# Kernel tuning notes

Measured on AMD Instinct MI355X. Metric: run time of the kernel, lower is better.

## Reference

```python
import jax, jax.numpy as jnp
import numpy as np

TOLX = 1e-12
TOLFUN = 1e-06
MAXITER = 1000
ALPHA = 1e-4
MIN_LAMBDA = 0.1
MAX_LAMBDA = 0.5
MAX_STEPS = 10  # fixed unroll budget; Newton converges in < 10 iterations for this problem
BS, NY = 200000, 8


def setup_inputs():
    key = jax.random.key(0)
    k1, k2, k3 = jax.random.split(key, 3)
    y0 = jax.random.normal(k1, (BS, NY), dtype=jnp.float32)
    W = 0.1 * jax.random.normal(k2, (NY, NY), dtype=jnp.float32)
    V = 0.1 * jax.random.normal(k3, (NY, NY), dtype=jnp.float32)
    dt = jnp.asarray(0.1, dtype=jnp.float32)
    t = jnp.asarray(1.0, dtype=jnp.float32)
    return {"y0": y0, "dt": dt, "t": t, "W": W, "V": V}


def _safe_div(n, d, eps=1e-30):
    ok = jnp.abs(d) > eps
    return jnp.where(ok, n / jnp.where(ok, d, 1.0), 0.0)


def _solver(y0, dt, t, W, V):
    bs, ny = y0.shape
    one = jnp.float32(1.0)

    def delta_S(tt, y):
        # test ODE right-hand side g(t, y): mildly nonlinear, acts per-sample
        return jnp.tanh(y @ W) @ V - 0.1 * y + 0.01 * jnp.sin(tt)

    def err(y):  # implicit-Euler residual, (bs, ny)
        return (y - y0) / dt - delta_S(t, y)

    def _err_single(yb, y0b):
        return (yb - y0b) / dt - (jnp.tanh(yb @ W) @ V - 0.1 * yb + 0.01 * jnp.sin(t))

    def batched_jac(y):
        # (bs, ny, ny): d err_b / d y_b; matches torch batch-diagonal of autograd jacobian
        return jax.vmap(jax.jacfwd(_err_single), in_axes=(0, 0))(y, y0)

    F0 = err(y0)
    jac0 = batched_jac(y0)
    rn0 = jnp.max(jnp.abs(F0), axis=1)
    fobj0 = jnp.einsum('bi,bi->b', F0, F0)

    state0 = dict(y=y0, yold=y0, F=F0, dy=jnp.zeros_like(y0), jac=jac0,
                  resnorm=rn0, resnorm0=100.0 * rn0,
                  lam=one, lam1=one, lam2=jnp.float32(0.5),
                  fold=fobj0, f2=fobj0, slope=jnp.zeros((bs,), y0.dtype),
                  lam_min=jnp.float32(0.0), niter=jnp.int32(0), exitflag=jnp.int32(1))

    def body(s, _):
        active = (((jnp.max(s['resnorm']) > TOLFUN) | (s['lam'] < 1.0))
                  & (s['exitflag'] >= 0) & (s['niter'] <= MAXITER))

        # --- lam == 1: fresh Newton direction, slope, objective ---
        is_newton = s['lam'] == 1.0
        recompute = jnp.max(_safe_div(s['resnorm'], s['resnorm0'])) > 0.2
        fresh_jac = batched_jac(s['y'])
        jac = jnp.where(is_newton & recompute, fresh_jac, s['jac'])
        dy_n = -jnp.linalg.solve(jac, s['F'][..., None])[..., 0]  # lstsq on square == solve
        gvec = jnp.einsum('bi,bij->bj', s['F'], jac)
        slope_n = jnp.einsum('bj,bj->b', gvec, dy_n)
        fold_n = jnp.einsum('bi,bi->b', s['F'], s['F'])
        lam_min_n = _safe_div(jnp.float32(TOLX),
                              jnp.max(jnp.abs(dy_n) / jnp.maximum(jnp.abs(s['y']), 1.0)))

        dy = jnp.where(is_newton, dy_n, s['dy'])
        slope = jnp.where(is_newton, slope_n, s['slope'])
        fold = jnp.where(is_newton, fold_n, s['fold'])
        yold = jnp.where(is_newton, s['y'], s['yold'])
        lam_min = jnp.where(is_newton, lam_min_n, s['lam_min'])
        niter = jnp.where(is_newton, s['niter'] + 1, s['niter'])

        brk = s['lam'] < lam_min            # -> exitflag = 2, freeze state
        bad = ~jnp.all(jnp.isfinite(dy))    # -> exitflag = -1, freeze state

        # --- trial step + trust-region line search ---
        lam = s['lam']
        y_new = yold + dy * lam
        F_new = err(y_new)
        f_obj = jnp.einsum('bi,bi->b', F_new, F_new)
        lam1 = lam
        lam2, f2 = s['lam2'], s['f2']

        backtrack = jnp.any(f_obj > fold + ALPHA * lam * slope)
        # quadratic model (first backtrack)
        lam_quad = jnp.min(_safe_div(-slope / 2.0, f_obj - fold - slope))
        # cubic model (subsequent backtracks)
        A = _safe_div(one, lam1 - lam2)
        inv1 = _safe_div(one, lam1 * lam1)
        inv2 = _safe_div(one, lam2 * lam2)
        B = jnp.stack([jnp.stack([inv1, -inv2]), jnp.stack([-lam2 * inv1, lam1 * inv2])])
        C = jnp.stack([f_obj - fold - lam1 * slope, f2 - fold - lam2 * slope])  # (2, bs)
        ab = A * (B @ C)
        a, b = ab[0], ab[1]
        disc = b * b - 3.0 * a * slope
        sq = jnp.sqrt(jnp.maximum(disc, 0.0))
        lam_tmp = jnp.where(jnp.all(a == 0.0), _safe_div(-slope, 2.0 * b),
                   jnp.where(jnp.any(disc < 0.0), MAX_LAMBDA * lam1,
                    jnp.where(jnp.any(b <= 0.0), _safe_div(-b + sq, 3.0 * a),
                     _safe_div(-slope, b + sq))))
        lam_cubic = jnp.min(jnp.minimum(lam_tmp, MAX_LAMBDA * lam1))
        lam_bt = jnp.where(lam == 1.0, lam_quad, lam_cubic)
        nanf = ~jnp.all(jnp.isfinite(f_obj))
        lam_new = jnp.where(backtrack, lam_bt, jnp.where(nanf, MAX_LAMBDA * lam1, one))

        cont = lam_new < 1.0  # retry with smaller lambda next iteration (the `continue` path)
        lam2_new = jnp.where(cont, lam1, lam2)
        f2_new = jnp.where(cont, f_obj, f2)
        lam_new = jnp.where(cont, jnp.maximum(lam_new, MIN_LAMBDA * lam1), lam_new)
        resnorm_new = jnp.where(cont, s['resnorm'], jnp.max(jnp.abs(F_new), axis=1))
        resnorm0_new = jnp.where(cont, s['resnorm0'], s['resnorm'])

        upd = active & (~brk) & (~bad)
        exitflag = jnp.where(active & brk, jnp.int32(2),
                    jnp.where(active & (~brk) & bad, jnp.int32(-1), s['exitflag']))
        sel = lambda new, old: jnp.where(upd, new, old)

        ns = dict(y=sel(y_new, s['y']), yold=sel(yold, s['yold']), F=sel(F_new, s['F']),
                  dy=sel(dy, s['dy']), jac=sel(jac, s['jac']),
                  resnorm=sel(resnorm_new, s['resnorm']), resnorm0=sel(resnorm0_new, s['resnorm0']),
                  lam=sel(lam_new, s['lam']), lam1=sel(lam1, s['lam1']), lam2=sel(lam2_new, s['lam2']),
                  fold=sel(fold, s['fold']), f2=sel(f2_new, s['f2']), slope=sel(slope, s['slope']),
                  lam_min=sel(lam_min, s['lam_min']),
                  niter=jnp.where(active, niter, s['niter']), exitflag=exitflag)
        return ns, None

    sN, _ = jax.lax.scan(body, state0, None, length=MAX_STEPS)
    return sN['y'], sN['F'], sN['exitflag']


def reference(y0, dt, t, W, V):
    y, F, exitflag = _solver(y0, dt, t, W, V)
    return (y, F, exitflag)
```

## Files before the change

### kernel.cpp

```cpp
#include <hip/hip_runtime.h>
#include <hip/hip_cooperative_groups.h>

namespace cg = cooperative_groups;

#define BSZ 200000
#define NSTEPS 10
#define TOLFUN_C 1e-6f
#define ALPHA_C 1e-4f

#define CNTHR 256
#define CNBLK 256
#define CNT   (CNBLK*CNTHR)
#define SPT   4
#define SLOTS (CNTHR*SPT)

#define FNTHR 256
#define FNBLK ((BSZ + FNTHR - 1)/FNTHR)

#define OFF_Y     ((size_t)0)
#define OFF_YOLD  ((size_t)BSZ*8)
#define OFF_DY    ((size_t)BSZ*16)
#define OFF_SJ    ((size_t)BSZ*24)
#define OFF_FOLD  ((size_t)BSZ*32)
#define OFF_SLOPE ((size_t)BSZ*33)
#define OFF_RESN  ((size_t)BSZ*34)
#define OFF_F2    ((size_t)BSZ*35)
#define OFF_TFO   ((size_t)BSZ*36)
#define OFF_TRN   ((size_t)BSZ*37)
#define OFF_R     ((size_t)BSZ*38)

#define RSTRIDE 64
#define NSLOT   9
#define R_TOT   (2 + NSTEPS*NSLOT)
#define KEY_MAX_IDENT 0x007FFFFFu
#define KEY_MIN_IDENT 0xFF800000u

static __device__ __forceinline__ float nanmax2(float a, float b){
    return (__builtin_isnan(a) || __builtin_isnan(b)) ? __builtin_nanf("") : fmaxf(a, b);
}
static __device__ __forceinline__ float nanmin2(float a, float b){
    return (__builtin_isnan(a) || __builtin_isnan(b)) ? __builtin_nanf("") : fminf(a, b);
}
static __device__ __forceinline__ float safe_div(float n, float d){
    return (fabsf(d) > 1e-30f) ? (n / d) : 0.0f;
}
static __device__ __forceinline__ unsigned fkey(float x){
    unsigned u = __float_as_uint(x);
    return (u & 0x80000000u) ? ~u : (u | 0x80000000u);
}
static __device__ __forceinline__ float funkey(unsigned u){
    return (u & 0x80000000u) ? __uint_as_float(u & 0x7FFFFFFFu) : __uint_as_float(~u);
}
static __device__ __forceinline__ unsigned fkey_max(float x){
    if (__builtin_isnan(x)) x = __uint_as_float(0x7FC00000u);
    return fkey(x);
}
static __device__ __forceinline__ unsigned fkey_min(float x){
    if (__builtin_isnan(x)) x = __uint_as_float(0xFFC00000u);
    return fkey(x);
}
static __device__ __forceinline__ void ld8(const float* p, float* v){
    float4 a = ((const float4*)p)[0], b = ((const float4*)p)[1];
    v[0]=a.x; v[1]=a.y; v[2]=a.z; v[3]=a.w; v[4]=b.x; v[5]=b.y; v[6]=b.z; v[7]=b.w;
}
static __device__ __forceinline__ void st8(float* p, const float* v){
    float4 a, b;
    a.x=v[0]; a.y=v[1]; a.z=v[2]; a.w=v[3];
    b.x=v[4]; b.y=v[5]; b.z=v[6]; b.w=v[7];
    ((float4*)p)[0]=a; ((float4*)p)[1]=b;
}
static __device__ __forceinline__ unsigned ldslot(const unsigned* p){
    return __hip_atomic_load(p, __ATOMIC_RELAXED, __HIP_MEMORY_SCOPE_AGENT);
}
static __device__ __forceinline__ void stslot(unsigned* p, unsigned v){
    __hip_atomic_store(p, v, __ATOMIC_RELAXED, __HIP_MEMORY_SCOPE_AGENT);
}

static __device__ __forceinline__ void computeFz(
    const float* yv, const float* y0v, float dt, float c0,
    const float* sW, const float* sV, float* Fo, float* zo)
{
    float u[8];
    #pragma unroll
    for (int k=0;k<8;k++){
        float acc = 0.f;
        #pragma unroll
        for (int m=0;m<8;m++) acc += yv[m]*sW[m*8+k];
        u[k]=acc;
    }
    #pragma unroll
    for (int k=0;k<8;k++) zo[k] = tanhf(u[k]);
    #pragma unroll
    for (int i=0;i<8;i++){
        float tv = 0.f;
        #pragma unroll
        for (int k=0;k<8;k++) tv += zo[k]*sV[k*8+i];
        Fo[i] = (yv[i]-y0v[i])/dt - ((tv - 0.1f*yv[i]) + c0);
    }
}

static __device__ __forceinline__ void devInit2(const float* y0v,
    float* yold, float* dy, float* sj,
    float& fold_o, float& slope_o, float& resn_o, float& f2_o,
    float dt, float c0, const float* sW, const float* sV,
    float& rn_red, float& rat_red)
{
    #pragma unroll
    for (int i=0;i<8;i++){ yold[i]=y0v[i]; dy[i]=0.f; }
    float Fv[8], z[8];
    computeFz(y0v, y0v, dt, c0, sW, sV, Fv, z);
    #pragma unroll
    for (int k=0;k<8;k++) sj[k] = 1.0f - z[k]*z[k];
    float fold = 0.f;
    #pragma unroll
    for (int i=0;i<8;i++) fold += Fv[i]*Fv[i];
    float rn0 = fabsf(Fv[0]);
    #pragma unroll
    for (int i=1;i<8;i++) rn0 = nanmax2(rn0, fabsf(Fv[i]));
    fold_o=fold; slope_o=0.f; resn_o=rn0; f2_o=fold;
    rn_red  = nanmax2(rn_red, rn0);
    rat_red = nanmax2(rat_red, safe_div(rn0, 100.0f*rn0));
}

static __device__ __forceinline__ void devA2(const float* y_cur, const float* y0v,
    float* yold, float* dy, float* sj, float& fold_o, float& slope_o,
    float dt, float invdt, float c0, const float* sW, const float* sV,
    bool recompute, float& gml, bool& nf)
{
    float Fv[8], z[8];
    computeFz(y_cur, y0v, dt, c0, sW, sV, Fv, z);
    if (recompute){
        #pragma unroll
        for (int k=0;k<8;k++) sj[k] = 1.0f - z[k]*z[k];
    }
    float J[8][8];
    #pragma unroll
    for (int j=0;j<8;j++){
        float zj[8];
        #pragma unroll
        for (int k=0;k<8;k++) zj[k] = sW[j*8+k]*sj[k];
        #pragma unroll
        for (int i=0;i<8;i++){
            float acc = 0.f;
            #pragma unroll
            for (int k=0;k<8;k++) acc += zj[k]*sV[k*8+i];
            J[i][j] = (i==j) ? (invdt - (acc - 0.1f)) : (0.0f - acc);
        }
    }
    float fold = 0.f;
    #pragma unroll
    for (int i=0;i<8;i++) fold += Fv[i]*Fv[i];
    float gv[8];
    #pragma unroll
    for (int j=0;j<8;j++){
        float acc = 0.f;
        #pragma unroll
        for (int i=0;i<8;i++) acc += Fv[i]*J[i][j];
        gv[j]=acc;
    }
    float x[8];
    #pragma unroll
    for (int i=0;i<8;i++) x[i]=Fv[i];
    #pragma unroll
    for (int c=0;c<8;c++){
        float ip = 1.0f / J[c][c];
        #pragma unroll
        for (int r2=c+1;r2<8;r2++){
            float m = J[r2][c]*ip;
            #pragma unroll
            for (int jj=c+1;jj<8;jj++) J[r2][jj] -= m*J[c][jj];
            x[r2] -= m*x[c];
        }
    }
    float wv[8];
    #pragma unroll
    for (int c=7;c>=0;c--){
        float acc = x[c];
        #pragma unroll
        for (int jj=c+1;jj<8;jj++) acc -= J[c][jj]*wv[jj];
        wv[c] = acc / J[c][c];
    }
    #pragma unroll
    for (int i=0;i<8;i++){
        yold[i] = y_cur[i];
        dy[i]   = -wv[i];
    }
    float slope = 0.f;
    #pragma unroll
    for (int j=0;j<8;j++) slope += gv[j]*dy[j];
    fold_o = fold; slope_o = slope;
    #pragma unroll
    for (int i=0;i<8;i++){
        float rr = fabsf(dy[i]) / nanmax2(fabsf(y_cur[i]), 1.0f);
        gml = nanmax2(gml, rr);
        nf = nf || !__builtin_isfinite(dy[i]);
    }
}

static __device__ __forceinline__ void devB2(const float* yold, const float* dy,
    const float* y0v, float foldv, float slopev, float resnv, float f2v,
    float dt, float c0, const float* sW, const float* sV, float lam, float lam2v,
    float& tfo_o, float& trn_o,
    bool& armijo, float& lq, bool& aNot0, bool& dN, bool& ble,
    float& mX, float& mZ, float& mW, bool& nanf, float& trnR, float& ratR)
{
    float yn[8];
    #pragma unroll
    for (int i=0;i<8;i++) yn[i] = yold[i] + dy[i]*lam;
    float Ft[8], z[8];
    computeFz(yn, y0v, dt, c0, sW, sV, Ft, z);
    float f_obj = 0.f;
    #pragma unroll
    for (int i=0;i<8;i++) f_obj += Ft[i]*Ft[i];
    float rn = fabsf(Ft[0]);
    #pragma unroll
    for (int i=1;i<8;i++) rn = nanmax2(rn, fabsf(Ft[i]));
    tfo_o = f_obj; trn_o = rn;
    armijo = armijo || (f_obj > (foldv + (ALPHA_C*lam)*slopev));
    lq = nanmin2(lq, safe_div((-slopev)*0.5f, (f_obj - foldv) - slopev));
    float lam1v = lam;
    float Af = safe_div(1.0f, lam1v - lam2v);
    float i1 = safe_div(1.0f, lam1v*lam1v);
    float i2 = safe_div(1.0f, lam2v*lam2v);
    float Cc0 = (f_obj - foldv) - lam1v*slopev;
    float Cc1 = (f2v   - foldv) - lam2v*slopev;
    float av = Af*(i1*Cc0 - i2*Cc1);
    float bv = Af*((-(lam2v*i1))*Cc0 + (lam1v*i2)*Cc1);
    float disc = bv*bv - (3.0f*av)*slopev;
    float dm = __builtin_isnan(disc) ? disc : fmaxf(disc, 0.0f);
    float sq = sqrtf(dm);
    aNot0 = aNot0 || (av != 0.0f);
    dN    = dN    || (disc < 0.0f);
    ble   = ble   || (bv <= 0.0f);
    mX = nanmin2(mX, safe_div(-slopev, 2.0f*bv));
    mZ = nanmin2(mZ, safe_div(-bv + sq, 3.0f*av));
    mW = nanmin2(mW, safe_div(-slopev, bv + sq));
    nanf = nanf || !__builtin_isfinite(f_obj);
    trnR = nanmax2(trnR, rn);
    ratR = nanmax2(ratR, safe_div(rn, resnv));
}

struct ScalarState {
    float lam, lam1, lam2, lam_min, maxrn, ratmax;
    int   niter, exitflag;
    bool  upd_prev, cont_prev;
};

static __device__ void advance(ScalarState& s, const unsigned* R, int j){
    const unsigned* r = R + (size_t)(2 + j*NSLOT)*RSTRIDE;
    unsigned v0 = ldslot(r + (size_t)0*RSTRIDE);
    unsigned v1 = ldslot(r + (size_t)1*RSTRIDE);
    unsigned v2 = ldslot(r + (size_t)2*RSTRIDE);
    unsigned v3 = ldslot(r + (size_t)3*RSTRIDE);
    unsigned v4 = ldslot(r + (size_t)4*RSTRIDE);
    unsigned v5 = ldslot(r + (size_t)5*RSTRIDE);
    unsigned v6 = ldslot(r + (size_t)6*RSTRIDE);
    unsigned v7 = ldslot(r + (size_t)7*RSTRIDE);
    unsigned v8 = ldslot(r + (size_t)8*RSTRIDE);
    bool active    = ((s.maxrn > TOLFUN_C) || (s.lam < 1.0f)) && (s.exitflag >= 0) && (s.niter <= 1000);
    bool is_newton = (s.lam == 1.0f);
    float lam_min_new = is_newton ? safe_div(1e-12f, funkey(v0)) : s.lam_min;
    bool brk = (s.lam < lam_min_new);
    bool bad = is_newton ? (v1 != 0u) : false;
    bool upd = active && !brk && !bad;
    int niter_new = active ? (is_newton ? s.niter + 1 : s.niter) : s.niter;
    int ef_new = s.exitflag;
    if (active && brk) ef_new = 2;
    else if (active && !brk && bad) ef_new = -1;
    bool cont = false;
    if (upd){
        float lam1c = s.lam;
        unsigned bm = v8;
        bool backtrack = (bm & 1u) != 0u;
        float lamq  = funkey(v2);
        bool allA0  = (bm & 2u) == 0u;
        bool anyDN  = (bm & 4u) != 0u;
        bool anyB0  = (bm & 8u) != 0u;
        float lam_tmp_min = allA0 ? funkey(v3)
                          : (anyDN ? (0.5f*lam1c)
                          : (anyB0 ? funkey(v4) : funkey(v5)));
        float lam_cubic = nanmin2(lam_tmp_min, 0.5f*lam1c);
        float lam_bt = (s.lam == 1.0f) ? lamq : lam_cubic;
        bool nanf = (bm & 16u) != 0u;
        float lam_new = backtrack ? lam_bt : (nanf ? 0.5f*lam1c : 1.0f);
        cont = (lam_new < 1.0f);
        float lam2_new = cont ? lam1c : s.lam2;
        if (cont) lam_new = nanmax2(lam_new, 0.1f*lam1c);
        float maxrn_new  = cont ? s.maxrn  : funkey(v6);
        float ratmax_new = cont ? s.ratmax : funkey(v7);
        s.lam = lam_new; s.lam1 = lam1c; s.lam2 = lam2_new;
        s.lam_min = lam_min_new; s.maxrn = maxrn_new; s.ratmax = ratmax_new;
    }
    s.niter = niter_new; s.exitflag = ef_new;
    s.upd_prev = upd; s.cont_prev = cont;
}

static __device__ ScalarState replayN(const unsigned* R, int n){
    ScalarState s;
    s.lam=1.0f; s.lam1=1.0f; s.lam2=0.5f; s.lam_min=0.0f;
    s.maxrn  = funkey(ldslot(&R[0]));
    s.ratmax = funkey(ldslot(&R[(size_t)1*RSTRIDE]));
    s.niter=0; s.exitflag=1; s.upd_prev=false; s.cont_prev=false;
    for (int j=0;j<n;++j) advance(s, R, j);
    return s;
}

__global__ __launch_bounds__(CNTHR, 1) void kFused(
    const float* __restrict__ y0g, const float* __restrict__ Wm, const float* __restrict__ Vm,
    const float* __restrict__ dtp, const float* __restrict__ tp,
    float* __restrict__ ws, float* __restrict__ out)
{
    cg::grid_group gridg = cg::this_grid();
    __shared__ float sW[64], sV[64];
    __shared__ float sSJ[8*SLOTS];
    __shared__ float redF[6][4];
    __shared__ unsigned redB[4];
    int t = threadIdx.x;
    if (t < 64) sW[t] = Wm[t];
    else if (t < 128) sV[t-64] = Vm[t-64];
    unsigned* R = (unsigned*)(ws + OFF_R);
    if (blockIdx.x == 0 && t < R_TOT){
        unsigned v;
        if (t < 2) v = KEY_MAX_IDENT;
        else {
            int off = (t - 2) % NSLOT;
            bool ismin = (off==2 || off==3 || off==4 || off==5);
            bool ismax = (off==0 || off==6 || off==7);
            v = ismin ? KEY_MIN_IDENT : (ismax ? KEY_MAX_IDENT : 0u);
        }
        stslot(&R[(size_t)t*RSTRIDE], v);
    }
    __syncthreads();
    gridg.sync();

    int gtid = blockIdx.x*CNTHR + t;
    float dt = *dtp, invdt = 1.0f/dt, c0 = 0.01f*sinf(*tp);

    bool  valid[SPT];
    float yold[SPT][8], dyv[SPT][8];
    float foldv[SPT], slopev[SPT], resnv[SPT], f2v[SPT], tfov[SPT], trnv[SPT];
    float lamc = 0.0f;

    float rn_red = -__builtin_inff(), rat_red = -__builtin_inff();
    #pragma unroll
    for (int q=0;q<SPT;q++){
        int sid = gtid + q*CNT;
        int slot = q*CNTHR + t;
        valid[q] = sid < BSZ;
        if (valid[q]){
            float y0v[8], sjl[8];
            ld8(y0g + (size_t)sid*8, y0v);
            devInit2(y0v, yold[q], dyv[q], sjl,
                     foldv[q], slopev[q], resnv[q], f2v[q],
                     dt, c0, sW, sV, rn_red, rat_red);
            #pragma unroll
            for (int i=0;i<8;i++) sSJ[i*SLOTS + slot] = sjl[i];
            tfov[q]=0.f; trnv[q]=0.f;
        } else {
            #pragma unroll
            for (int i=0;i<8;i++){ sSJ[i*SLOTS + slot]=0; yold[q][i]=0; dyv[q][i]=0; }
            foldv[q]=0; slopev[q]=0; resnv[q]=0; f2v[q]=0; tfov[q]=0; trnv[q]=0;
        }
    }
    #pragma unroll
    for (int o=32;o>=1;o>>=1){
        rn_red  = nanmax2(rn_red,  __shfl_xor(rn_red,  o, 64));
        rat_red = nanmax2(rat_red, __shfl_xor(rat_red, o, 64));
    }
    {
        int w = t >> 6;
        if ((t & 63) == 0){ redF[0][w] = rn_red; redF[1][w] = rat_red; }
        __syncthreads();
        if (t == 0){
            float a = redF[0][0];
            #pragma unroll
            for (int w2=1;w2<4;w2++) a = nanmax2(a, redF[0][w2]);
            atomicMax(&R[0], fkey_max(a));
        } else if (t == 1){
            float b = redF[1][0];
            #pragma unroll
            for (int w2=1;w2<4;w2++) b = nanmax2(b, redF[1][w2]);
            atomicMax(&R[(size_t)1*RSTRIDE], fkey_max(b));
        }
    }
    gridg.sync();

    ScalarState S;
    S.lam=1.0f; S.lam1=1.0f; S.lam2=0.5f; S.lam_min=0.0f;
    S.maxrn  = funkey(ldslot(&R[0]));
    S.ratmax = funkey(ldslot(&R[(size_t)1*RSTRIDE]));
    S.niter=0; S.exitflag=1; S.upd_prev=false; S.cont_prev=false;

    #pragma unroll 1
    for (int k=1; k<=NSTEPS; ++k){
        if (S.upd_prev){
            lamc = S.lam1;
            #pragma unroll
            for (int q=0;q<SPT;q++){
                if (!valid[q]) continue;
                if (S.cont_prev) f2v[q]  = tfov[q];
                else             resnv[q] = trnv[q];
            }
        }
        bool active    = ((S.maxrn > TOLFUN_C) || (S.lam < 1.0f)) && (S.exitflag >= 0) && (S.niter <= 1000);
        bool is_newton = (S.lam == 1.0f);
        unsigned* r = R + (size_t)(2 + (k-1)*NSLOT)*RSTRIDE;

        if (active && is_newton){
            bool recompute = (S.ratmax > 0.2f);
            float gml = -__builtin_inff(); bool nf = false;
            #pragma unroll
            for (int q=0;q<SPT;q++){
                if (!valid[q]) continue;
                int sid = gtid + q*CNT;
                int slot = q*CNTHR + t;
                float y_cur[8], y0v[8], sjl[8];
                ld8(y0g + (size_t)sid*8, y0v);
                #pragma unroll
                for (int i=0;i<8;i++){
                    y_cur[i] = yold[q][i] + dyv[q][i]*lamc;
                    sjl[i]   = sSJ[i*SLOTS + slot];
                }
                devA2(y_cur, y0v, yold[q], dyv[q], sjl, foldv[q], slopev[q],
                      dt, invdt, c0, sW, sV, recompute, gml, nf);
                if (recompute){
                    #pragma unroll
                    for (int i=0;i<8;i++) sSJ[i*SLOTS + slot] = sjl[i];
                }
            }
            lamc = 0.0f;
            #pragma unroll
            for (int o=32;o>=1;o>>=1) gml = nanmax2(gml, __shfl_xor(gml, o, 64));
            unsigned long long anym = __ballot(nf ? 1 : 0);
            int w = t >> 6;
            if ((t & 63) == 0){ redF[0][w] = gml; redB[w] = anym ? 1u : 0u; }
            __syncthreads();
            if (t == 0){
                float v = redF[0][0];
                #pragma unroll
                for (int w2=1;w2<4;w2++) v = nanmax2(v, redF[0][w2]);
                atomicMax(&r[0], fkey_max(v));
            } else if (t == 1){
                unsigned bm = redB[0]|redB[1]|redB[2]|redB[3];
                if (bm) atomicOr(&r[(size_t)1*RSTRIDE], 1u);
            }
            __syncthreads();
        }

        if (active){
            float lam = S.lam, lam2v = S.lam2;
            bool armijo=false, aNot0=false, dN=false, ble=false, nanf=false;
            float lq=__builtin_inff(), mX=__builtin_inff(), mZ=__builtin_inff(), mW=__builtin_inff();
            float trnR=-__builtin_inff(), ratR=-__builtin_inff();
            #pragma unroll
            for (int q=0;q<SPT;q++){
                if (!valid[q]) continue;
                int sid = gtid + q*CNT;
                float y0v[8];
                ld8(y0g + (size_t)sid*8, y0v);
                devB2(yold[q], dyv[q], y0v, foldv[q], slopev[q], resnv[q], f2v[q],
                      dt, c0, sW, sV, lam, lam2v, tfov[q], trnv[q],
                      armijo, lq, aNot0, dN, ble, mX, mZ, mW, nanf, trnR, ratR);
            }
            #pragma unroll
            for (int o=32;o>=1;o>>=1){
                lq   = nanmin2(lq,   __shfl_xor(lq,   o, 64));
                mX   = nanmin2(mX,   __shfl_xor(mX,   o, 64));
                mZ   = nanmin2(mZ,   __shfl_xor(mZ,   o, 64));
                mW   = nanmin2(mW,   __shfl_xor(mW,   o, 64));
                trnR = nanmax2(trnR, __shfl_xor(trnR, o, 64));
                ratR = nanmax2(ratR, __shfl_xor(ratR, o, 64));
            }
            unsigned long long bArm = __ballot(armijo ? 1 : 0);
            unsigned long long bA0  = __ballot(aNot0  ? 1 : 0);
            unsigned long long bDN  = __ballot(dN     ? 1 : 0);
            unsigned long long bB0  = __ballot(ble    ? 1 : 0);
            unsigned long long bNF  = __ballot(nanf   ? 1 : 0);
            int w = t >> 6;
            if ((t & 63) == 0){
                redF[0][w]=lq; redF[1][w]=mX; redF[2][w]=mZ; redF[3][w]=mW;
                redF[4][w]=trnR; redF[5][w]=ratR;
                redB[w] = (bArm?1u:0u) | (bA0?2u:0u) | (bDN?4u:0u) | (bB0?8u:0u) | (bNF?16u:0u);
            }
            __syncthreads();
            if (t < 6){
                float v = redF[t][0];
                bool ismin = (t < 4);
                #pragma unroll
                for (int w2=1;w2<4;w2++) v = ismin ? nanmin2(v, redF[t][w2]) : nanmax2(v, redF[t][w2]);
                unsigned* p = &r[(size_t)(t + 2)*RSTRIDE];
                if (ismin) atomicMin(p, fkey_min(v));
                else       atomicMax(p, fkey_max(v));
            } else if (t == 6){
                unsigned bm = redB[0]|redB[1]|redB[2]|redB[3];
                if (bm) atomicOr(&r[(size_t)8*RSTRIDE], bm);
            }
        }

        gridg.sync();
        advance(S, R, k-1);
    }

    if (S.upd_prev) lamc = S.lam1;
    #pragma unroll
    for (int q=0;q<SPT;q++){
        if (!valid[q]) continue;
        int sid = gtid + q*CNT;
        float yf[8], y0v[8];
        ld8(y0g + (size_t)sid*8, y0v);
        #pragma unroll
        for (int i=0;i<8;i++) yf[i] = yold[q][i] + dyv[q][i]*lamc;
        st8(out + (size_t)sid*8, yf);
        float Fv[8], z[8];
        computeFz(yf, y0v, dt, c0, sW, sV, Fv, z);
        st8(out + (size_t)BSZ*8 + (size_t)sid*8, Fv);
    }
    if (gtid == 0) out[(size_t)BSZ*16] = (float)S.exitflag;
}

__global__ void kPre(unsigned* __restrict__ R){
    int i = threadIdx.x;
    if (i >= R_TOT) return;
    unsigned v;
    if (i < 2) v = KEY_MAX_IDENT;
    else {
        int off = (i - 2) % NSLOT;
        bool ismin = (off==2 || off==3 || off==4 || off==5);
        bool ismax = (off==0 || off==6 || off==7);
        v = ismin ? KEY_MIN_IDENT : (ismax ? KEY_MAX_IDENT : 0u);
    }
    R[(size_t)i*RSTRIDE] = v;
}

__global__ __launch_bounds__(FNTHR) void fInit(
    const float* __restrict__ y0g, const float* __restrict__ Wm, const float* __restrict__ Vm,
    const float* __restrict__ dtp, const float* __restrict__ tp, float* __restrict__ ws)
{
    __shared__ float sW[64], sV[64];
    __shared__ float red[2][4];
    int t = threadIdx.x;
    if (t < 64) sW[t] = Wm[t];
    else if (t < 128) sV[t-64] = Vm[t-64];
    __syncthreads();
    unsigned* R = (unsigned*)(ws + OFF_R);
    int tid = blockIdx.x*FNTHR + t;
    bool valid = tid < BSZ;
    float dt = *dtp, c0 = 0.01f*sinf(*tp);
    float rn_red = -__builtin_inff(), rat_red = -__builtin_inff();
    if (valid){
        float y0v[8], yo[8], dv[8], sj[8], fold, slope, resn, f2;
        ld8(y0g + (size_t)tid*8, y0v);
        devInit2(y0v, yo, dv, sj, fold, slope, resn, f2, dt, c0, sW, sV, rn_red, rat_red);
        st8(ws+OFF_Y   +(size_t)tid*8, y0v);
        st8(ws+OFF_YOLD+(size_t)tid*8, yo);
        st8(ws+OFF_DY  +(size_t)tid*8, dv);
        st8(ws+OFF_SJ  +(size_t)tid*8, sj);
        ws[OFF_FOLD+tid]=fold; ws[OFF_SLOPE+tid]=slope;
        ws[OFF_RESN+tid]=resn; ws[OFF_F2+tid]=f2;
        ws[OFF_TFO+tid]=0.f;   ws[OFF_TRN+tid]=0.f;
    }
    #pragma unroll
    for (int o=32;o>=1;o>>=1){
        rn_red  = nanmax2(rn_red,  __shfl_xor(rn_red,  o, 64));
        rat_red = nanmax2(rat_red, __shfl_xor(rat_red, o, 64));
    }
    int w = t >> 6;
    if ((t & 63) == 0){ red[0][w]=rn_red; red[1][w]=rat_red; }
    __syncthreads();
    if (t == 0){
        float a = red[0][0];
        for (int w2=1;w2<4;w2++) a = nanmax2(a, red[0][w2]);
        atomicMax(&R[0], fkey_max(a));
    } else if (t == 1){
        float b = red[1][0];
        for (int w2=1;w2<4;w2++) b = nanmax2(b, red[1][w2]);
        atomicMax(&R[(size_t)1*RSTRIDE], fkey_max(b));
    }
}

__global__ __launch_bounds__(FNTHR) void fStep(
    const float* __restrict__ y0g, const float* __restrict__ Wm, const float* __restrict__ Vm,
    const float* __restrict__ dtp, const float* __restrict__ tp,
    float* __restrict__ ws, int step)
{
    __shared__ float sW[64], sV[64];
    __shared__ float redF[6][4];
    __shared__ unsigned redB[4];
    int t = threadIdx.x;
    if (t < 64) sW[t] = Wm[t];
    else if (t < 128) sV[t-64] = Vm[t-64];
    __syncthreads();
    unsigned* R = (unsigned*)(ws + OFF_R);
    ScalarState S = replayN(R, step-1);
    bool active    = ((S.maxrn > TOLFUN_C) || (S.lam < 1.0f)) && (S.exitflag >= 0) && (S.niter <= 1000);
    bool is_newton = (S.lam == 1.0f);
    if (!S.upd_prev && !active) return;

    int tid = blockIdx.x*FNTHR + t;
    bool valid = tid < BSZ;
    float dt = *dtp, invdt = 1.0f/dt, c0 = 0.01f*sinf(*tp);
    unsigned* r = R + (size_t)(2 + (step-1)*NSLOT)*RSTRIDE;

    float y0v[8], yv[8], yo[8], dv[8], sj[8], fold=0, slope=0, resn=0, f2=0;
    if (valid){
        ld8(y0g + (size_t)tid*8, y0v);
        ld8(ws+OFF_Y   +(size_t)tid*8, yv);
        ld8(ws+OFF_YOLD+(size_t)tid*8, yo);
        ld8(ws+OFF_DY  +(size_t)tid*8, dv);
        ld8(ws+OFF_SJ  +(size_t)tid*8, sj);
        fold=ws[OFF_FOLD+tid]; slope=ws[OFF_SLOPE+tid];
        resn=ws[OFF_RESN+tid]; f2=ws[OFF_F2+tid];
        if (S.upd_prev){
            #pragma unroll
            for (int i=0;i<8;i++) yv[i] = yo[i] + dv[i]*S.lam1;
            st8(ws+OFF_Y+(size_t)tid*8, yv);
            if (S.cont_prev){ f2 = ws[OFF_TFO+tid];  ws[OFF_F2+tid]   = f2; }
            else            { resn = ws[OFF_TRN+tid]; ws[OFF_RESN+tid] = resn; }
        }
    }
    if (!active) return;

    if (is_newton){
        bool recompute = (S.ratmax > 0.2f);
        float gml = -__builtin_inff(); bool nf = false;
        if (valid){
            devA2(yv, y0v, yo, dv, sj, fold, slope, dt, invdt, c0, sW, sV, recompute, gml, nf);
            st8(ws+OFF_YOLD+(size_t)tid*8, yo);
            st8(ws+OFF_DY  +(size_t)tid*8, dv);
            if (recompute) st8(ws+OFF_SJ+(size_t)tid*8, sj);
            ws[OFF_FOLD+tid]  = fold;
            ws[OFF_SLOPE+tid] = slope;
        }
        #pragma unroll
        for (int o=32;o>=1;o>>=1) gml = nanmax2(gml, __shfl_xor(gml, o, 64));
        unsigned long long anym = __ballot(nf ? 1 : 0);
        int w = t >> 6;
        if ((t & 63) == 0){ redF[0][w] = gml; redB[w] = anym ? 1u : 0u; }
        __syncthreads();
        if (t == 0){
            float v = redF[0][0];
            for (int w2=1;w2<4;w2++) v = nanmax2(v, redF[0][w2]);
            atomicMax(&r[0], fkey_max(v));
        } else if (t == 1){
            unsigned bm = redB[0]|redB[1]|redB[2]|redB[3];
            if (bm) atomicOr(&r[(size_t)1*RSTRIDE], 1u);
        }
        __syncthreads();
    }

    {
        float lam = S.lam, lam2v = S.lam2;
        bool armijo=false, aNot0=false, dN=false, ble=false, nanf=false;
        float lq=__builtin_inff(), mX=__builtin_inff(), mZ=__builtin_inff(), mW=__builtin_inff();
        float trnR=-__builtin_inff(), ratR=-__builtin_inff();
        if (valid){
            float tfo, trn;
            devB2(yo, dv, y0v, fold, slope, resn, f2, dt, c0, sW, sV, lam, lam2v,
                  tfo, trn, armijo, lq, aNot0, dN, ble, mX, mZ, mW, nanf, trnR, ratR);
            ws[OFF_TFO+tid] = tfo;
            ws[OFF_TRN+tid] = trn;
        }
        #pragma unroll
        for (int o=32;o>=1;o>>=1){
            lq   = nanmin2(lq,   __shfl_xor(lq,   o, 64));
            mX   = nanmin2(mX,   __shfl_xor(mX,   o, 64));
            mZ   = nanmin2(mZ,   __shfl_xor(mZ,   o, 64));
            mW   = nanmin2(mW,   __shfl_xor(mW,   o, 64));
            trnR = nanmax2(trnR, __shfl_xor(trnR, o, 64));
            ratR = nanmax2(ratR, __shfl_xor(ratR, o, 64));
        }
        unsigned long long bArm = __ballot(armijo ? 1 : 0);
        unsigned long long bA0  = __ballot(aNot0  ? 1 : 0);
        unsigned long long bDN  = __ballot(dN     ? 1 : 0);
        unsigned long long bB0  = __ballot(ble    ? 1 : 0);
        unsigned long long bNF  = __ballot(nanf   ? 1 : 0);
        int w = t >> 6;
        if ((t & 63) == 0){
            redF[0][w]=lq; redF[1][w]=mX; redF[2][w]=mZ; redF[3][w]=mW;
            redF[4][w]=trnR; redF[5][w]=ratR;
            redB[w] = (bArm?1u:0u) | (bA0?2u:0u) | (bDN?4u:0u) | (bB0?8u:0u) | (bNF?16u:0u);
        }
        __syncthreads();
        if (t < 6){
            float v = redF[t][0];
            bool ismin = (t < 4);
            for (int w2=1;w2<4;w2++) v = ismin ? nanmin2(v, redF[t][w2]) : nanmax2(v, redF[t][w2]);
            unsigned* p = &r[(size_t)(t + 2)*RSTRIDE];
            if (ismin) atomicMin(p, fkey_min(v));
            else       atomicMax(p, fkey_max(v));
        } else if (t == 6){
            unsigned bm = redB[0]|redB[1]|redB[2]|redB[3];
            if (bm) atomicOr(&r[(size_t)8*RSTRIDE], bm);
        }
    }
}

__global__ __launch_bounds__(FNTHR) void fOut(
    const float* __restrict__ y0g, const float* __restrict__ Wm, const float* __restrict__ Vm,
    const float* __restrict__ dtp, const float* __restrict__ tp,
    const float* __restrict__ ws, float* __restrict__ out)
{
    __shared__ float sW[64], sV[64];
    int t = threadIdx.x;
    if (t < 64) sW[t] = Wm[t];
    else if (t < 128) sV[t-64] = Vm[t-64];
    __syncthreads();
    const unsigned* R = (const unsigned*)(ws + OFF_R);
    ScalarState S = replayN(R, NSTEPS);
    int tid = blockIdx.x*FNTHR + t;
    float dt = *dtp, c0 = 0.01f*sinf(*tp);
    if (tid < BSZ){
        float y0v[8], yv[8];
        ld8(y0g + (size_t)tid*8, y0v);
        ld8(ws+OFF_Y+(size_t)tid*8, yv);
        if (S.upd_prev){
            float yo[8], dv[8];
            ld8(ws+OFF_YOLD+(size_t)tid*8, yo);
            ld8(ws+OFF_DY  +(size_t)tid*8, dv);
            #pragma unroll
            for (int i=0;i<8;i++) yv[i] = yo[i] + dv[i]*S.lam1;
        }
        st8(out + (size_t)tid*8, yv);
        float Fv[8], z[8];
        computeFz(yv, y0v, dt, c0, sW, sV, Fv, z);
        st8(out + (size_t)BSZ*8 + (size_t)tid*8, Fv);
    }
    if (blockIdx.x == 0 && t == 0) out[(size_t)BSZ*16] = (float)S.exitflag;
}

extern "C" void kernel_launch(void* const* d_in, const int* in_sizes, int n_in,
                              void* d_out, int out_size, void* d_ws, size_t ws_size,
                              hipStream_t stream)
{
    const float* y0g = (const float*)d_in[0];
    const float* dtp = (const float*)d_in[1];
    const float* tp  = (const float*)d_in[2];
    const float* Wm  = (const float*)d_in[3];
    const float* Vm  = (const float*)d_in[4];
    float* ws   = (float*)d_ws;
    float* outp = (float*)d_out;

    int occ = 0;
    hipError_t qrc = hipOccupancyMaxActiveBlocksPerMultiprocessor(
        &occ, (const void*)kFused, CNTHR, 0);
    bool try_coop = (qrc == hipSuccess && occ >= 1);

    hipError_t rc = hipErrorUnknown;
    if (try_coop){
        void* args[] = {(void*)&y0g, (void*)&Wm, (void*)&Vm, (void*)&dtp, (void*)&tp,
                        (void*)&ws, (void*)&outp};
        rc = hipLaunchCooperativeKernel((const void*)kFused, dim3(CNBLK), dim3(CNTHR),
                                        args, 0, stream);
    }
    if (rc != hipSuccess){
        hipLaunchKernelGGL(kPre, dim3(1), dim3(128), 0, stream, (unsigned*)(ws + OFF_R));
        hipLaunchKernelGGL(fInit, dim3(FNBLK), dim3(FNTHR), 0, stream, y0g, Wm, Vm, dtp, tp, ws);
        for (int s = 1; s <= NSTEPS; ++s)
            hipLaunchKernelGGL(fStep, dim3(FNBLK), dim3(FNTHR), 0, stream, y0g, Wm, Vm, dtp, tp, ws, s);
        hipLaunchKernelGGL(fOut, dim3(FNBLK), dim3(FNTHR), 0, stream, y0g, Wm, Vm, dtp, tp, ws, outp);
    }
}
```

Baseline: 446.9 us.

## Cache trial residuals in LDS to skip recomputation and double the cooperative grid

The line-search residual computed in phase B is now kept in shared memory and reused as the Newton residual in phase A and for the final output. This removes a full tanh/matvec evaluation per sample per step and the extra y0 reloads. The cooperative grid also doubles to 512 blocks with 2 samples per thread and launch bounds of 2 blocks per CU, trading per-thread work for occupancy. The extra LDS buffer and the register limit could spill, and the cooperative-launch check now requires two resident blocks per CU.

```diff
diff --git a/kernel.cpp b/kernel.cpp
--- a/kernel.cpp
+++ b/kernel.cpp
@@ -9,9 +9,9 @@
 #define ALPHA_C 1e-4f
 
 #define CNTHR 256
-#define CNBLK 256
+#define CNBLK 512
 #define CNT   (CNBLK*CNTHR)
-#define SPT   4
+#define SPT   2
 #define SLOTS (CNTHR*SPT)
 
 #define FNTHR 256
@@ -100,26 +100,107 @@
 }
 
 static __device__ __forceinline__ void devInit2(const float* y0v,
-    float* yold, float* dy, float* sj,
+    float* yold, float* dy, float* sj, float* F_out,
     float& fold_o, float& slope_o, float& resn_o, float& f2_o,
     float dt, float c0, const float* sW, const float* sV,
     float& rn_red, float& rat_red)
 {
     #pragma unroll
     for (int i=0;i<8;i++){ yold[i]=y0v[i]; dy[i]=0.f; }
-    float Fv[8], z[8];
-    computeFz(y0v, y0v, dt, c0, sW, sV, Fv, z);
+    float z[8];
+    computeFz(y0v, y0v, dt, c0, sW, sV, F_out, z);
     #pragma unroll
     for (int k=0;k<8;k++) sj[k] = 1.0f - z[k]*z[k];
     float fold = 0.f;
     #pragma unroll
-    for (int i=0;i<8;i++) fold += Fv[i]*Fv[i];
-    float rn0 = fabsf(Fv[0]);
-    #pragma unroll
-    for (int i=1;i<8;i++) rn0 = nanmax2(rn0, fabsf(Fv[i]));
+    for (int i=0;i<8;i++) fold += F_out[i]*F_out[i];
+    float rn0 = fabsf(F_out[0]);
+    #pragma unroll
+    for (int i=1;i<8;i++) rn0 = nanmax2(rn0, fabsf(F_out[i]));
     fold_o=fold; slope_o=0.f; resn_o=rn0; f2_o=fold;
     rn_red  = nanmax2(rn_red, rn0);
     rat_red = nanmax2(rat_red, safe_div(rn0, 100.0f*rn0));
+}
+
+static __device__ __forceinline__ void devA3(const float* y_cur, const float* Fv,
+    float* yold, float* dy, float* sj, float& fold_o, float& slope_o,
+    float invdt, const float* sW, const float* sV,
+    bool recompute, float& gml, bool& nf)
+{
+    if (recompute){
+        float u[8];
+        #pragma unroll
+        for (int k=0;k<8;k++){
+            float acc = 0.f;
+            #pragma unroll
+            for (int m=0;m<8;m++) acc += y_cur[m]*sW[m*8+k];
+            u[k]=acc;
+        }
+        #pragma unroll
+        for (int k=0;k<8;k++){ float z = tanhf(u[k]); sj[k] = 1.0f - z*z; }
+    }
+    float J[8][8];
+    #pragma unroll
+    for (int j=0;j<8;j++){
+        float zj[8];
+        #pragma unroll
+        for (int k=0;k<8;k++) zj[k] = sW[j*8+k]*sj[k];
+        #pragma unroll
+        for (int i=0;i<8;i++){
+            float acc = 0.f;
+            #pragma unroll
+            for (int k=0;k<8;k++) acc += zj[k]*sV[k*8+i];
+            J[i][j] = (i==j) ? (invdt - (acc - 0.1f)) : (0.0f - acc);
+        }
+    }
+    float fold = 0.f;
+    #pragma unroll
+    for (int i=0;i<8;i++) fold += Fv[i]*Fv[i];
+    float gv[8];
+    #pragma unroll
+    for (int j=0;j<8;j++){
+        float acc = 0.f;
+        #pragma unroll
+        for (int i=0;i<8;i++) acc += Fv[i]*J[i][j];
+        gv[j]=acc;
+    }
+    float x[8];
+    #pragma unroll
+    for (int i=0;i<8;i++) x[i]=Fv[i];
+    #pragma unroll
+    for (int c=0;c<8;c++){
+        float ip = 1.0f / J[c][c];
+        #pragma unroll
+        for (int r2=c+1;r2<8;r2++){
+            float m = J[r2][c]*ip;
+            #pragma unroll
+            for (int jj=c+1;jj<8;jj++) J[r2][jj] -= m*J[c][jj];
+            x[r2] -= m*x[c];
+        }
+    }
+    float wv[8];
+    #pragma unroll
+    for (int c=7;c>=0;c--){
+        float acc = x[c];
+        #pragma unroll
+        for (int jj=c+1;jj<8;jj++) acc -= J[c][jj]*wv[jj];
+        wv[c] = acc / J[c][c];
+    }
+    #pragma unroll
+    for (int i=0;i<8;i++){
+        yold[i] = y_cur[i];
+        dy[i]   = -wv[i];
+    }
+    float slope = 0.f;
+    #pragma unroll
+    for (int j=0;j<8;j++) slope += gv[j]*dy[j];
+    fold_o = fold; slope_o = slope;
+    #pragma unroll
+    for (int i=0;i<8;i++){
+        float rr = fabsf(dy[i]) / nanmax2(fabsf(y_cur[i]), 1.0f);
+        gml = nanmax2(gml, rr);
+        nf = nf || !__builtin_isfinite(dy[i]);
+    }
 }
 
 static __device__ __forceinline__ void devA2(const float* y_cur, const float* y0v,
@@ -133,81 +214,20 @@
         #pragma unroll
         for (int k=0;k<8;k++) sj[k] = 1.0f - z[k]*z[k];
     }
-    float J[8][8];
-    #pragma unroll
-    for (int j=0;j<8;j++){
-        float zj[8];
-        #pragma unroll
-        for (int k=0;k<8;k++) zj[k] = sW[j*8+k]*sj[k];
-        #pragma unroll
-        for (int i=0;i<8;i++){
-            float acc = 0.f;
-            #pragma unroll
-            for (int k=0;k<8;k++) acc += zj[k]*sV[k*8+i];
-            J[i][j] = (i==j) ? (invdt - (acc - 0.1f)) : (0.0f - acc);
-        }
-    }
-    float fold = 0.f;
-    #pragma unroll
-    for (int i=0;i<8;i++) fold += Fv[i]*Fv[i];
-    float gv[8];
-    #pragma unroll
-    for (int j=0;j<8;j++){
-        float acc = 0.f;
-        #pragma unroll
-        for (int i=0;i<8;i++) acc += Fv[i]*J[i][j];
-        gv[j]=acc;
-    }
-    float x[8];
-    #pragma unroll
-    for (int i=0;i<8;i++) x[i]=Fv[i];
-    #pragma unroll
-    for (int c=0;c<8;c++){
-        float ip = 1.0f / J[c][c];
-        #pragma unroll
-        for (int r2=c+1;r2<8;r2++){
-            float m = J[r2][c]*ip;
-            #pragma unroll
-            for (int jj=c+1;jj<8;jj++) J[r2][jj] -= m*J[c][jj];
-            x[r2] -= m*x[c];
-        }
-    }
-    float wv[8];
-    #pragma unroll
-    for (int c=7;c>=0;c--){
-        float acc = x[c];
-        #pragma unroll
-        for (int jj=c+1;jj<8;jj++) acc -= J[c][jj]*wv[jj];
-        wv[c] = acc / J[c][c];
-    }
-    #pragma unroll
-    for (int i=0;i<8;i++){
-        yold[i] = y_cur[i];
-        dy[i]   = -wv[i];
-    }
-    float slope = 0.f;
-    #pragma unroll
-    for (int j=0;j<8;j++) slope += gv[j]*dy[j];
-    fold_o = fold; slope_o = slope;
-    #pragma unroll
-    for (int i=0;i<8;i++){
-        float rr = fabsf(dy[i]) / nanmax2(fabsf(y_cur[i]), 1.0f);
-        gml = nanmax2(gml, rr);
-        nf = nf || !__builtin_isfinite(dy[i]);
-    }
+    devA3(y_cur, Fv, yold, dy, sj, fold_o, slope_o, invdt, sW, sV, false, gml, nf);
 }
 
 static __device__ __forceinline__ void devB2(const float* yold, const float* dy,
     const float* y0v, float foldv, float slopev, float resnv, float f2v,
     float dt, float c0, const float* sW, const float* sV, float lam, float lam2v,
-    float& tfo_o, float& trn_o,
+    float* Ft, float& tfo_o, float& trn_o,
     bool& armijo, float& lq, bool& aNot0, bool& dN, bool& ble,
     float& mX, float& mZ, float& mW, bool& nanf, float& trnR, float& ratR)
 {
     float yn[8];
     #pragma unroll
     for (int i=0;i<8;i++) yn[i] = yold[i] + dy[i]*lam;
-    float Ft[8], z[8];
+    float z[8];
     computeFz(yn, y0v, dt, c0, sW, sV, Ft, z);
     float f_obj = 0.f;
     #pragma unroll
@@ -305,7 +325,7 @@
     return s;
 }
 
-__global__ __launch_bounds__(CNTHR, 1) void kFused(
+__global__ __launch_bounds__(CNTHR, 2) void kFused(
     const float* __restrict__ y0g, const float* __restrict__ Wm, const float* __restrict__ Vm,
     const float* __restrict__ dtp, const float* __restrict__ tp,
     float* __restrict__ ws, float* __restrict__ out)
@@ -313,6 +333,7 @@
     cg::grid_group gridg = cg::this_grid();
     __shared__ float sW[64], sV[64];
     __shared__ float sSJ[8*SLOTS];
+    __shared__ float sFT[8*SLOTS];
     __shared__ float redF[6][4];
     __shared__ unsigned redB[4];
     int t = threadIdx.x;
@@ -337,7 +358,7 @@
     float dt = *dtp, invdt = 1.0f/dt, c0 = 0.01f*sinf(*tp);
 
     bool  valid[SPT];
-    float yold[SPT][8], dyv[SPT][8];
+    float yold[SPT][8], dyv[SPT][8], Fp[SPT][8];
     float foldv[SPT], slopev[SPT], resnv[SPT], f2v[SPT], tfov[SPT], trnv[SPT];
     float lamc = 0.0f;
 
@@ -350,7 +371,7 @@
         if (valid[q]){
             float y0v[8], sjl[8];
             ld8(y0g + (size_t)sid*8, y0v);
-            devInit2(y0v, yold[q], dyv[q], sjl,
+            devInit2(y0v, yold[q], dyv[q], sjl, Fp[q],
                      foldv[q], slopev[q], resnv[q], f2v[q],
                      dt, c0, sW, sV, rn_red, rat_red);
             #pragma unroll
@@ -358,7 +379,7 @@
             tfov[q]=0.f; trnv[q]=0.f;
         } else {
             #pragma unroll
-            for (int i=0;i<8;i++){ sSJ[i*SLOTS + slot]=0; yold[q][i]=0; dyv[q][i]=0; }
+            for (int i=0;i<8;i++){ sSJ[i*SLOTS + slot]=0; yold[q][i]=0; dyv[q][i]=0; Fp[q][i]=0; }
             foldv[q]=0; slopev[q]=0; resnv[q]=0; f2v[q]=0; tfov[q]=0; trnv[q]=0;
         }
     }
@@ -398,6 +419,9 @@
             #pragma unroll
             for (int q=0;q<SPT;q++){
                 if (!valid[q]) continue;
+                int slot = q*CNTHR + t;
+                #pragma unroll
+                for (int i=0;i<8;i++) Fp[q][i] = sFT[i*SLOTS + slot];
                 if (S.cont_prev) f2v[q]  = tfov[q];
                 else             resnv[q] = trnv[q];
             }
@@ -412,17 +436,15 @@
             #pragma unroll
             for (int q=0;q<SPT;q++){
                 if (!valid[q]) continue;
-                int sid = gtid + q*CNT;
                 int slot = q*CNTHR + t;
-                float y_cur[8], y0v[8], sjl[8];
-                ld8(y0g + (size_t)sid*8, y0v);
+                float y_cur[8], sjl[8];
                 #pragma unroll
                 for (int i=0;i<8;i++){
                     y_cur[i] = yold[q][i] + dyv[q][i]*lamc;
                     sjl[i]   = sSJ[i*SLOTS + slot];
                 }
-                devA2(y_cur, y0v, yold[q], dyv[q], sjl, foldv[q], slopev[q],
-                      dt, invdt, c0, sW, sV, recompute, gml, nf);
+                devA3(y_cur, Fp[q], yold[q], dyv[q], sjl, foldv[q], slopev[q],
+                      invdt, sW, sV, recompute, gml, nf);
                 if (recompute){
                     #pragma unroll
                     for (int i=0;i<8;i++) sSJ[i*SLOTS + slot] = sjl[i];
@@ -456,11 +478,14 @@
             for (int q=0;q<SPT;q++){
                 if (!valid[q]) continue;
                 int sid = gtid + q*CNT;
-                float y0v[8];
+                int slot = q*CNTHR + t;
+                float y0v[8], Ftl[8];
                 ld8(y0g + (size_t)sid*8, y0v);
                 devB2(yold[q], dyv[q], y0v, foldv[q], slopev[q], resnv[q], f2v[q],
-                      dt, c0, sW, sV, lam, lam2v, tfov[q], trnv[q],
+                      dt, c0, sW, sV, lam, lam2v, Ftl, tfov[q], trnv[q],
                       armijo, lq, aNot0, dN, ble, mX, mZ, mW, nanf, trnR, ratR);
+                #pragma unroll
+                for (int i=0;i<8;i++) sFT[i*SLOTS + slot] = Ftl[i];
             }
             #pragma unroll
             for (int o=32;o>=1;o>>=1){
@@ -501,19 +526,25 @@
         advance(S, R, k-1);
     }
 
-    if (S.upd_prev) lamc = S.lam1;
+    if (S.upd_prev){
+        lamc = S.lam1;
+        #pragma unroll
+        for (int q=0;q<SPT;q++){
+            if (!valid[q]) continue;
+            int slot = q*CNTHR + t;
+            #pragma unroll
+            for (int i=0;i<8;i++) Fp[q][i] = sFT[i*SLOTS + slot];
+        }
+    }
     #pragma unroll
     for (int q=0;q<SPT;q++){
         if (!valid[q]) continue;
         int sid = gtid + q*CNT;
-        float yf[8], y0v[8];
-        ld8(y0g + (size_t)sid*8, y0v);
+        float yf[8];
         #pragma unroll
         for (int i=0;i<8;i++) yf[i] = yold[q][i] + dyv[q][i]*lamc;
         st8(out + (size_t)sid*8, yf);
-        float Fv[8], z[8];
-        computeFz(yf, y0v, dt, c0, sW, sV, Fv, z);
-        st8(out + (size_t)BSZ*8 + (size_t)sid*8, Fv);
+        st8(out + (size_t)BSZ*8 + (size_t)sid*8, Fp[q]);
     }
     if (gtid == 0) out[(size_t)BSZ*16] = (float)S.exitflag;
 }
@@ -548,9 +579,9 @@
     float dt = *dtp, c0 = 0.01f*sinf(*tp);
     float rn_red = -__builtin_inff(), rat_red = -__builtin_inff();
     if (valid){
-        float y0v[8], yo[8], dv[8], sj[8], fold, slope, resn, f2;
+        float y0v[8], yo[8], dv[8], sj[8], Fv[8], fold, slope, resn, f2;
         ld8(y0g + (size_t)tid*8, y0v);
-        devInit2(y0v, yo, dv, sj, fold, slope, resn, f2, dt, c0, sW, sV, rn_red, rat_red);
+        devInit2(y0v, yo, dv, sj, Fv, fold, slope, resn, f2, dt, c0, sW, sV, rn_red, rat_red);
         st8(ws+OFF_Y   +(size_t)tid*8, y0v);
         st8(ws+OFF_YOLD+(size_t)tid*8, yo);
         st8(ws+OFF_DY  +(size_t)tid*8, dv);
@@ -654,9 +685,9 @@
         float lq=__builtin_inff(), mX=__builtin_inff(), mZ=__builtin_inff(), mW=__builtin_inff();
         float trnR=-__builtin_inff(), ratR=-__builtin_inff();
         if (valid){
-            float tfo, trn;
+            float tfo, trn, Ftl[8];
             devB2(yo, dv, y0v, fold, slope, resn, f2, dt, c0, sW, sV, lam, lam2v,
-                  tfo, trn, armijo, lq, aNot0, dN, ble, mX, mZ, mW, nanf, trnR, ratR);
+                  Ftl, tfo, trn, armijo, lq, aNot0, dN, ble, mX, mZ, mW, nanf, trnR, ratR);
             ws[OFF_TFO+tid] = tfo;
             ws[OFF_TRN+tid] = trn;
         }
@@ -743,7 +774,7 @@
     int occ = 0;
     hipError_t qrc = hipOccupancyMaxActiveBlocksPerMultiprocessor(
         &occ, (const void*)kFused, CNTHR, 0);
-    bool try_coop = (qrc == hipSuccess && occ >= 1);
+    bool try_coop = (qrc == hipSuccess && occ * 256 >= CNBLK);
 
     hipError_t rc = hipErrorUnknown;
     if (try_coop){
```

Measured after the change: 444.5 us. No clear change (-0.5%).
